# Kernel tuning notes

Hardware: AMD Instinct MI355X
Metric: run time of the kernel (lower is better)

## Reference

```python
import jax, jax.numpy as jnp
import numpy as np

EPS = 1e-5  # InstanceNorm2d default eps


def setup_inputs() -> dict:
    key = jax.random.key(0)
    ks = jax.random.split(key, 5)
    B, T, C, N, H = 4, 8, 256, 196, 4
    s = 1.0 / np.sqrt(C)
    return {
        "emb": jax.random.normal(ks[0], (B, T, C, N), dtype=jnp.float32),
        "Wq": jax.random.normal(ks[1], (H, C, C), dtype=jnp.float32) * s,
        "Wk": jax.random.normal(ks[2], (H, C, C), dtype=jnp.float32) * s,
        "Wv": jax.random.normal(ks[3], (H, C, C), dtype=jnp.float32) * s,
        "Wo": jax.random.normal(ks[4], (C, C), dtype=jnp.float32) * s,
    }


def reference(emb, Wq, Wk, Wv, Wo):
    B, T, C, N = emb.shape
    S = T * N  # KV_size
    # emb.permute(0,1,3,2).view(B, T*N, C)
    x = jnp.transpose(emb, (0, 1, 3, 2)).reshape(B, S, C)
    # per-head full-width Linear projections (nn.Linear: y = x @ W.T)
    Q = jnp.einsum("bsc,hdc->bhsd", x, Wq)  # [B,H,S,C]
    K = jnp.einsum("bsc,hdc->bhsd", x, Wk)
    V = jnp.einsum("bsc,hdc->bhsd", x, Wv)
    scores = jnp.einsum("bhsd,bhtd->bhst", Q, K) / jnp.sqrt(jnp.float32(S))
    # InstanceNorm2d over each [S,S] map per (batch, head), no affine, biased var
    mean = jnp.mean(scores, axis=(-2, -1), keepdims=True)
    var = jnp.var(scores, axis=(-2, -1), keepdims=True)
    normed = (scores - mean) * jax.lax.rsqrt(var + EPS)
    probs = jax.nn.softmax(normed, axis=-1)  # attn_dropout: eval-mode identity
    ctx = jnp.einsum("bhst,bhtd->bhsd", probs, V)  # [B,H,S,C]
    ctx = jnp.mean(ctx, axis=1)  # mean over heads -> [B,S,C]
    O1 = jnp.einsum("bsc,dc->bsd", ctx, Wo)  # out Linear; proj_dropout identity
    # .view(-1, num_frames, num_channels, num_patches) on contiguous [B, T*N, C]
    return O1.reshape(B, T, C, N)
```

## Files before the change

kernel.cpp:

```cpp
#include <hip/hip_runtime.h>
#include <stdint.h>

typedef unsigned short u16;

#define Bb 4
#define Hh 4
#define Tt 8
#define Cc 256
#define NP 196
#define Ss 1568
#define SCALE_S 0.0252538136f
#define LST 32
#define KC 64
#define NCH 25
#define LPP 72

typedef __attribute__((ext_vector_type(4))) float floatx4;
typedef __attribute__((ext_vector_type(8))) short shortx8;

__device__ __forceinline__ float bf2f(u16 u) {
    union { unsigned u; float f; } v; v.u = ((unsigned)u) << 16; return v.f;
}
__device__ __forceinline__ u16 f2bf(float f) {
    union { float f; unsigned u; } v; v.f = f;
    unsigned r = v.u + 0x7FFFu + ((v.u >> 16) & 1u);
    return (u16)(r >> 16);
}

typedef const __attribute__((address_space(1))) void* gas1_t;
typedef __attribute__((address_space(3))) void* las3_t;
__device__ __forceinline__ void gld16(const void* g, void* l) {
    __builtin_amdgcn_global_load_lds((gas1_t)g, (las3_t)l, 16, 0, 0);
}

__global__ __launch_bounds__(256) void k_convall(const float* __restrict__ Wq,
                                                 const float* __restrict__ Wk,
                                                 const float* __restrict__ Wv,
                                                 const float* __restrict__ Wo,
                                                 u16* __restrict__ dst) {
    const int NW = Hh * Cc * Cc;
    int i = blockIdx.x * 256 + threadIdx.x;
    float v;
    if (i < NW) v = Wq[i];
    else if (i < 2 * NW) v = Wk[i - NW];
    else if (i < 3 * NW) v = Wv[i - 2 * NW];
    else if (i < 3 * NW + Cc * Cc) v = Wo[i - 3 * NW];
    else return;
    dst[i] = f2bf(v);
}

__device__ __forceinline__ void mfma_step(const u16* As, const u16* Bs, int lane,
                                          int wm, int wn, floatx4 acc[4][4]) {
    const int r15 = lane & 15;
    const int kq  = (lane >> 4) << 3;
    shortx8 a[4], b[4];
#pragma unroll
    for (int i = 0; i < 4; ++i)
        a[i] = *(const shortx8*)(As + (wm * 64 + i * 16 + r15) * LST + kq);
#pragma unroll
    for (int j = 0; j < 4; ++j)
        b[j] = *(const shortx8*)(Bs + (wn * 64 + j * 16 + r15) * LST + kq);
#pragma unroll
    for (int i = 0; i < 4; ++i)
#pragma unroll
        for (int j = 0; j < 4; ++j)
            acc[i][j] = __builtin_amdgcn_mfma_f32_16x16x32_bf16(a[i], b[j], acc[i][j], 0, 0, 0);
}

__device__ __forceinline__ void gemm_bt_core(const u16* A, const u16* Bm, int lda, int ldb,
                                             int mbase, int mlast, int nbase, int nlast,
                                             int KD, u16* As, u16* Bs, floatx4 acc[4][4]) {
    int tid = threadIdx.x;
    int lane = tid & 63, wave = tid >> 6, wm = wave >> 1, wn = wave & 1;
    int row0 = tid >> 2, row1 = 64 + row0;
    int cole = (tid & 3) << 3;
    int ga0 = mbase + row0; ga0 = ga0 <= mlast ? ga0 : mlast;
    int ga1 = mbase + row1; ga1 = ga1 <= mlast ? ga1 : mlast;
    int gb0 = nbase + row0; gb0 = gb0 <= nlast ? gb0 : nlast;
    int gb1 = nbase + row1; gb1 = gb1 <= nlast ? gb1 : nlast;
    const u16* pa0 = A  + (size_t)ga0 * lda + cole;
    const u16* pa1 = A  + (size_t)ga1 * lda + cole;
    const u16* pb0 = Bm + (size_t)gb0 * ldb + cole;
    const u16* pb1 = Bm + (size_t)gb1 * ldb + cole;
    shortx8 xa0 = *(const shortx8*)(pa0),      xa1 = *(const shortx8*)(pa1);
    shortx8 xb0 = *(const shortx8*)(pb0),      xb1 = *(const shortx8*)(pb1);
    shortx8 ya0 = *(const shortx8*)(pa0 + 32), ya1 = *(const shortx8*)(pa1 + 32);
    shortx8 yb0 = *(const shortx8*)(pb0 + 32), yb1 = *(const shortx8*)(pb1 + 32);
    for (int k0 = 0; k0 < KD; k0 += 64) {
        __syncthreads();
        *(shortx8*)(As + row0 * LST + cole) = xa0;
        *(shortx8*)(As + row1 * LST + cole) = xa1;
        *(shortx8*)(Bs + row0 * LST + cole) = xb0;
        *(shortx8*)(Bs + row1 * LST + cole) = xb1;
        int kp = k0 + 64;
        if (kp < KD) {
            xa0 = *(const shortx8*)(pa0 + kp); xa1 = *(const shortx8*)(pa1 + kp);
            xb0 = *(const shortx8*)(pb0 + kp); xb1 = *(const shortx8*)(pb1 + kp);
        }
        __syncthreads();
        mfma_step(As, Bs, lane, wm, wn, acc);
        if (k0 + 32 < KD) {
            __syncthreads();
            *(shortx8*)(As + row0 * LST + cole) = ya0;
            *(shortx8*)(As + row1 * LST + cole) = ya1;
            *(shortx8*)(Bs + row0 * LST + cole) = yb0;
            *(shortx8*)(Bs + row1 * LST + cole) = yb1;
            int kq2 = k0 + 96;
            if (kq2 < KD) {
                ya0 = *(const shortx8*)(pa0 + kq2); ya1 = *(const shortx8*)(pa1 + kq2);
                yb0 = *(const shortx8*)(pb0 + kq2); yb1 = *(const shortx8*)(pb1 + kq2);
            }
            __syncthreads();
            mfma_step(As, Bs, lane, wm, wn, acc);
        }
    }
}

__global__ void k_transpose(const float* __restrict__ emb, u16* __restrict__ x) {
    __shared__ u16 tile[32][33];
    int bt = blockIdx.z;
    int c0 = blockIdx.y * 32, n0 = blockIdx.x * 32;
    const float* src = emb + (size_t)bt * Cc * NP;
#pragma unroll
    for (int rr = 0; rr < 32; rr += 8) {
        int c = c0 + threadIdx.y + rr;
        int n = n0 + threadIdx.x;
        u16 v = 0;
        if (n < NP) v = f2bf(src[(size_t)c * NP + n]);
        tile[threadIdx.y + rr][threadIdx.x] = v;
    }
    __syncthreads();
    int b = bt / Tt, t = bt % Tt;
    u16* dst = x + ((size_t)b * Ss + (size_t)t * NP) * Cc;
#pragma unroll
    for (int rr = 0; rr < 32; rr += 8) {
        int n = n0 + threadIdx.y + rr;
        int c = c0 + threadIdx.x;
        if (n < NP) dst[(size_t)n * Cc + c] = tile[threadIdx.x][threadIdx.y + rr];
    }
}

__global__ __launch_bounds__(256) void k_qkv(const u16* __restrict__ x,
                                             const u16* __restrict__ Wall,
                                             u16* __restrict__ Q, u16* __restrict__ Kb,
                                             u16* __restrict__ Vt, u16* __restrict__ Qt,
                                             u16* __restrict__ Kt, float* __restrict__ cs) {
    __shared__ __align__(16) u16 As[128 * LST], Bs[128 * LST];
    floatx4 acc[4][4];
#pragma unroll
    for (int i = 0; i < 4; ++i)
#pragma unroll
        for (int j = 0; j < 4; ++j) acc[i][j] = (floatx4)(0.f);
    int z = blockIdx.z;
    int qkv = z >> 4, bh = z & 15, b = bh >> 2, h = bh & 3;
    const u16* A = x + (size_t)b * Ss * Cc;
    const u16* W = Wall + (size_t)qkv * Hh * Cc * Cc + (size_t)h * Cc * Cc;
    int mbase = blockIdx.y * 128, nbase = blockIdx.x * 128;
    gemm_bt_core(A, W, Cc, Cc, mbase, Ss - 1, nbase, Cc - 1, Cc, As, Bs, acc);

    int tid = threadIdx.x, lane = tid & 63, wave = tid >> 6, wm = wave >> 1, wn = wave & 1;
    int rq = (lane >> 4) << 2, cn = lane & 15;
    if (qkv < 2) {
        u16* outr = (qkv == 0 ? Q : Kb) + (size_t)bh * Ss * Cc;
        u16* outt = (qkv == 0 ? Qt : Kt) + (size_t)bh * Cc * Ss;
#pragma unroll
        for (int i = 0; i < 4; ++i) {
            int m0 = mbase + wm * 64 + i * 16 + rq;
#pragma unroll
            for (int j = 0; j < 4; ++j) {
                int n = nbase + wn * 64 + j * 16 + cn;
                ushort4 v;
                v.x = f2bf(acc[i][j][0]); v.y = f2bf(acc[i][j][1]);
                v.z = f2bf(acc[i][j][2]); v.w = f2bf(acc[i][j][3]);
#pragma unroll
                for (int r = 0; r < 4; ++r) {
                    int m = m0 + r;
                    if (m < Ss) outr[(size_t)m * Cc + n] = f2bf(acc[i][j][r]);
                }
                if (m0 < Ss) *(ushort4*)(outt + (size_t)n * Ss + m0) = v;
            }
        }
#pragma unroll
        for (int j = 0; j < 4; ++j) {
            float s = 0.f;
#pragma unroll
            for (int i = 0; i < 4; ++i) {
                int m0 = mbase + wm * 64 + i * 16 + rq;
#pragma unroll
                for (int r = 0; r < 4; ++r)
                    if (m0 + r < Ss) s += acc[i][j][r];
            }
            s += __shfl_xor(s, 16); s += __shfl_xor(s, 32);
            if ((lane >> 4) == 0) {
                int n = nbase + wn * 64 + j * 16 + cn;
                atomicAdd(&cs[(size_t)(qkv * 16 + bh) * Cc + n], s);
            }
        }
    } else {
        u16* out = Vt + (size_t)bh * Cc * Ss;
#pragma unroll
        for (int i = 0; i < 4; ++i) {
            int m0 = mbase + wm * 64 + i * 16 + rq;
            if (m0 < Ss) {
#pragma unroll
                for (int j = 0; j < 4; ++j) {
                    int n = nbase + wn * 64 + j * 16 + cn;
                    ushort4 v;
                    v.x = f2bf(acc[i][j][0]); v.y = f2bf(acc[i][j][1]);
                    v.z = f2bf(acc[i][j][2]); v.w = f2bf(acc[i][j][3]);
                    *(ushort4*)(out + (size_t)n * Ss + m0) = v;
                }
            }
        }
    }
}

__global__ __launch_bounds__(256) void k_gram(const u16* __restrict__ Qt,
                                              const u16* __restrict__ Kt,
                                              float* __restrict__ Gp) {
    __shared__ __align__(16) u16 As[128 * LST], Bs[128 * LST];
    floatx4 acc[4][4];
#pragma unroll
    for (int i = 0; i < 4; ++i)
#pragma unroll
        for (int j = 0; j < 4; ++j) acc[i][j] = (floatx4)(0.f);
    int z = blockIdx.z;
    int qk = z >> 6, rem = z & 63, bh = rem >> 2, ks = rem & 3;
    int kstart = ks * 384;
    int klen = (ks == 3) ? 416 : 384;
    const u16* T = (qk ? Kt : Qt) + (size_t)bh * Cc * Ss + kstart;
    int mbase = blockIdx.y * 128, nbase = blockIdx.x * 128;
    gemm_bt_core(T, T, Ss, Ss, mbase, Cc - 1, nbase, Cc - 1, klen, As, Bs, acc);

    int tid = threadIdx.x, lane = tid & 63, wave = tid >> 6, wm = wave >> 1, wn = wave & 1;
    int rq = (lane >> 4) << 2, cn = lane & 15;
    float* o = Gp + (size_t)z * (Cc * Cc);
#pragma unroll
    for (int i = 0; i < 4; ++i) {
        int mb = mbase + wm * 64 + i * 16 + rq;
#pragma unroll
        for (int j = 0; j < 4; ++j) {
            int n = nbase + wn * 64 + j * 16 + cn;
#pragma unroll
            for (int r = 0; r < 4; ++r)
                o[(size_t)(mb + r) * Cc + n] = acc[i][j][r];
        }
    }
}

__global__ __launch_bounds__(256) void k_dot(const float* __restrict__ Gp,
                                             const float* __restrict__ cs,
                                             float* __restrict__ stats) {
    __shared__ float red[4];
    int bh = blockIdx.y;
    int tid = threadIdx.x, lane = tid & 63, wave = tid >> 6;
    const size_t CC2 = (size_t)Cc * Cc;
    size_t bq = (size_t)(bh << 2) * CC2;
    size_t bk = (size_t)(64 + (bh << 2)) * CC2;
    float s2 = 0.f;
    int e0 = blockIdx.x * 8192;
#pragma unroll 4
    for (int i = 0; i < 32; ++i) {
        int e = e0 + i * 256 + tid;
        float gq = Gp[bq + e] + Gp[bq + CC2 + e] + Gp[bq + 2 * CC2 + e] + Gp[bq + 3 * CC2 + e];
        float gk = Gp[bk + e] + Gp[bk + CC2 + e] + Gp[bk + 2 * CC2 + e] + Gp[bk + 3 * CC2 + e];
        s2 += gq * gk;
    }
#pragma unroll
    for (int mk = 1; mk <= 32; mk <<= 1) s2 += __shfl_xor(s2, mk);
    __syncthreads();
    if (lane == 0) red[wave] = s2;
    __syncthreads();
    if (tid == 0)
        atomicAdd(&stats[bh * 4 + 1], (red[0] + red[1] + red[2] + red[3]) * (SCALE_S * SCALE_S));
    if (blockIdx.x == 0) {
        float s1 = cs[(size_t)bh * Cc + tid] * cs[(size_t)(16 + bh) * Cc + tid];
#pragma unroll
        for (int mk = 1; mk <= 32; mk <<= 1) s1 += __shfl_xor(s1, mk);
        __syncthreads();
        if (lane == 0) red[wave] = s1;
        __syncthreads();
        if (tid == 0)
            atomicAdd(&stats[bh * 4 + 0], (red[0] + red[1] + red[2] + red[3]) * SCALE_S);
    }
}

__global__ __launch_bounds__(256, 2) void k_fused(const u16* __restrict__ Q,
                                                  const u16* __restrict__ Kb,
                                                  const u16* __restrict__ Vt,
                                                  const float* __restrict__ stats,
                                                  float* __restrict__ ctxm) {
    extern __shared__ u16 smem[];
    u16* Kls = smem;
    u16* Ps  = smem + 32768;
    float* rsp = (float*)((char*)smem + 74752);
    float* rs2 = rsp + 128;

    int L = blockIdx.x;
    int xcd = L & 7, idx = L >> 3;
    int bh = xcd + 8 * (idx / 25);
    int mt = idx % 25;
    int mbase = mt * 64;

    float inv  = 1.f / ((float)Ss * (float)Ss);
    float mean = stats[bh * 4] * inv;
    float var  = fmaxf(stats[bh * 4 + 1] * inv - mean * mean, 0.f);
    float istd = rsqrtf(var + 1e-5f);
    float aa   = istd * 1.44269504f;
    float aas  = aa * SCALE_S;
    float bb   = -mean * aa;

    const u16* Qp = Q  + (size_t)bh * Ss * Cc;
    const u16* Kp = Kb + (size_t)bh * Ss * Cc;
    const u16* Vp = Vt + (size_t)bh * Cc * Ss;

    int tid = threadIdx.x, lane = tid & 63, wv = tid >> 6;
    const int r15 = lane & 15;
    const int g   = lane >> 4;
    const int kq  = g << 3;
    const int prow = g << 2;
    const int wqm = wv >> 1, wqn = wv & 1;
    const int swz = (r15 & 7) << 4;

    shortx8 Qa[8][2];
#pragma unroll
    for (int kk = 0; kk < 8; ++kk)
#pragma unroll
        for (int i = 0; i < 2; ++i) {
            int row = mbase + wqm * 32 + i * 16 + r15;
            row = row < Ss ? row : Ss - 1;
            Qa[kk][i] = *(const shortx8*)(Qp + (size_t)row * Cc + kk * 32 + kq);
        }

#pragma unroll
    for (int pass = 0; pass < 8; ++pass) {
        int rb = pass * 4 + wv;
        int r2 = rb * 2 + (lane >> 5);
        int colb = (lane & 31) << 4;
        int scol = colb ^ ((r2 & 7) << 4);
        gld16((const char*)Kp + (size_t)r2 * 512 + scol, Kls + rb * 512);
    }
    __syncthreads();

    floatx4 acc[4][4];
#pragma unroll
    for (int i = 0; i < 4; ++i)
#pragma unroll
        for (int j = 0; j < 4; ++j) acc[i][j] = (floatx4)(0.f);
    float rsum[2][4];
    rsum[0][0] = rsum[0][1] = rsum[0][2] = rsum[0][3] = 0.f;
    rsum[1][0] = rsum[1][1] = rsum[1][2] = rsum[1][3] = 0.f;

    int cur = 0;
    for (int c = 0; c < NCH; ++c) {
        int kc = c * KC;
        const u16* Kcur = Kls + cur * 16384;
        if (c + 1 < NCH) {
            int kc1 = kc + KC;
            u16* Knxt = Kls + (cur ^ 1) * 16384;
#pragma unroll
            for (int pass = 0; pass < 8; ++pass) {
                int rb = pass * 4 + wv;
                int r2 = rb * 2 + (lane >> 5);
                int colb = (lane & 31) << 4;
                int scol = colb ^ ((r2 & 7) << 4);
                int grow = kc1 + r2; grow = grow < Ss ? grow : 0;
                gld16((const char*)Kp + (size_t)grow * 512 + scol, Knxt + rb * 512);
            }
        }
        shortx8 vf[2][4];
#pragma unroll
        for (int kk2 = 0; kk2 < 2; ++kk2)
#pragma unroll
            for (int nj = 0; nj < 4; ++nj) {
                int vr = wv * 64 + nj * 16 + r15;
                int vc = kc + kk2 * 32 + kq;
                vc = (vc + 8 <= Ss) ? vc : 0;
                vf[kk2][nj] = *(const shortx8*)(Vp + (size_t)vr * Ss + vc);
            }
        floatx4 accs[2][2];
        accs[0][0] = (floatx4)(0.f); accs[0][1] = (floatx4)(0.f);
        accs[1][0] = (floatx4)(0.f); accs[1][1] = (floatx4)(0.f);
        const int cb = g << 4;
#pragma unroll
        for (int kk = 0; kk < 8; ++kk) {
            int cbx = (kk * 64 + cb) ^ swz;
            shortx8 b0 = *(const shortx8*)((const char*)Kcur + (wqn * 32 + r15) * 512 + cbx);
            shortx8 b1 = *(const shortx8*)((const char*)Kcur + (wqn * 32 + 16 + r15) * 512 + cbx);
            accs[0][0] = __builtin_amdgcn_mfma_f32_16x16x32_bf16(Qa[kk][0], b0, accs[0][0], 0, 0, 0);
            accs[1][0] = __builtin_amdgcn_mfma_f32_16x16x32_bf16(Qa[kk][1], b0, accs[1][0], 0, 0, 0);
            accs[0][1] = __builtin_amdgcn_mfma_f32_16x16x32_bf16(Qa[kk][0], b1, accs[0][1], 0, 0, 0);
            accs[1][1] = __builtin_amdgcn_mfma_f32_16x16x32_bf16(Qa[kk][1], b1, accs[1][1], 0, 0, 0);
        }
#pragma unroll
        for (int j = 0; j < 2; ++j) {
            bool valid = (kc + wqn * 32 + j * 16 + r15) < Ss;
#pragma unroll
            for (int i = 0; i < 2; ++i)
#pragma unroll
                for (int r = 0; r < 4; ++r) {
                    float ex = valid ? exp2f(accs[i][j][r] * aas + bb) : 0.f;
                    accs[i][j][r] = ex;
                    rsum[i][r] += ex;
                }
        }
        __syncthreads();
#pragma unroll
        for (int i = 0; i < 2; ++i)
#pragma unroll
            for (int j = 0; j < 2; ++j)
#pragma unroll
                for (int r = 0; r < 4; ++r)
                    Ps[(wqm * 32 + i * 16 + prow + r) * LPP + wqn * 32 + j * 16 + r15] =
                        f2bf(accs[i][j][r]);
        __syncthreads();
#pragma unroll
        for (int kk2 = 0; kk2 < 2; ++kk2) {
            shortx8 pa_[4];
#pragma unroll
            for (int i2 = 0; i2 < 4; ++i2)
                pa_[i2] = *(const shortx8*)(Ps + (i2 * 16 + r15) * LPP + kk2 * 32 + kq);
#pragma unroll
            for (int i2 = 0; i2 < 4; ++i2)
#pragma unroll
                for (int nj = 0; nj < 4; ++nj)
                    acc[i2][nj] = __builtin_amdgcn_mfma_f32_16x16x32_bf16(
                        pa_[i2], vf[kk2][nj], acc[i2][nj], 0, 0, 0);
        }
        cur ^= 1;
    }

#pragma unroll
    for (int i = 0; i < 2; ++i)
#pragma unroll
        for (int r = 0; r < 4; ++r) {
            float v = rsum[i][r];
            v += __shfl_xor(v, 1); v += __shfl_xor(v, 2);
            v += __shfl_xor(v, 4); v += __shfl_xor(v, 8);
            if (r15 == 0) rsp[wqn * 64 + wqm * 32 + i * 16 + prow + r] = v;
        }
    __syncthreads();
    if (tid < 64) rs2[tid] = rsp[tid] + rsp[64 + tid];
    __syncthreads();

    int b = bh >> 2;
    float* outp = ctxm + (size_t)b * Ss * Cc;
#pragma unroll
    for (int i2 = 0; i2 < 4; ++i2) {
#pragma unroll
        for (int r = 0; r < 4; ++r) {
            int ml = i2 * 16 + prow + r;
            int m = mbase + ml;
            if (m < Ss) {
                float invs = 0.25f / rs2[ml];
#pragma unroll
                for (int nj = 0; nj < 4; ++nj) {
                    int n = wv * 64 + nj * 16 + r15;
                    atomicAdd(&outp[(size_t)m * Cc + n], acc[i2][nj][r] * invs);
                }
            }
        }
    }
}

__global__ __launch_bounds__(256) void k_out(const float* __restrict__ ctxm,
                                             const u16* __restrict__ Wo, float* __restrict__ out) {
    __shared__ __align__(16) u16 As[128 * LST], Bs[128 * LST];
    floatx4 acc[4][4];
#pragma unroll
    for (int i = 0; i < 4; ++i)
#pragma unroll
        for (int j = 0; j < 4; ++j) acc[i][j] = (floatx4)(0.f);
    int b = blockIdx.z;
    const float* A = ctxm + (size_t)b * Ss * Cc;
    int mbase = blockIdx.y * 128, nbase = blockIdx.x * 128;
    int tid = threadIdx.x, lane = tid & 63, wave = tid >> 6, wm = wave >> 1, wn = wave & 1;
    int row0 = tid >> 2, row1 = 64 + row0;
    int cole = (tid & 3) << 3;
    int ga0 = mbase + row0; ga0 = ga0 <= Ss - 1 ? ga0 : Ss - 1;
    int ga1 = mbase + row1; ga1 = ga1 <= Ss - 1 ? ga1 : Ss - 1;
    const float* pa0 = A + (size_t)ga0 * Cc + cole;
    const float* pa1 = A + (size_t)ga1 * Cc + cole;
    const u16* pb0 = Wo + (size_t)(nbase + row0 <= Cc - 1 ? nbase + row0 : Cc - 1) * Cc + cole;
    const u16* pb1 = Wo + (size_t)(nbase + row1 <= Cc - 1 ? nbase + row1 : Cc - 1) * Cc + cole;
    float4 a00 = *(const float4*)(pa0), a01 = *(const float4*)(pa0 + 4);
    float4 a10 = *(const float4*)(pa1), a11 = *(const float4*)(pa1 + 4);
    shortx8 vb0 = *(const shortx8*)(pb0);
    shortx8 vb1 = *(const shortx8*)(pb1);
    for (int k0 = 0; k0 < Cc; k0 += 32) {
        shortx8 o0, o1;
        o0[0] = (short)f2bf(a00.x); o0[1] = (short)f2bf(a00.y); o0[2] = (short)f2bf(a00.z); o0[3] = (short)f2bf(a00.w);
        o0[4] = (short)f2bf(a01.x); o0[5] = (short)f2bf(a01.y); o0[6] = (short)f2bf(a01.z); o0[7] = (short)f2bf(a01.w);
        o1[0] = (short)f2bf(a10.x); o1[1] = (short)f2bf(a10.y); o1[2] = (short)f2bf(a10.z); o1[3] = (short)f2bf(a10.w);
        o1[4] = (short)f2bf(a11.x); o1[5] = (short)f2bf(a11.y); o1[6] = (short)f2bf(a11.z); o1[7] = (short)f2bf(a11.w);
        __syncthreads();
        *(shortx8*)(As + row0 * LST + cole) = o0;
        *(shortx8*)(As + row1 * LST + cole) = o1;
        *(shortx8*)(Bs + row0 * LST + cole) = vb0;
        *(shortx8*)(Bs + row1 * LST + cole) = vb1;
        int k1 = k0 + 32;
        if (k1 < Cc) {
            a00 = *(const float4*)(pa0 + k1); a01 = *(const float4*)(pa0 + k1 + 4);
            a10 = *(const float4*)(pa1 + k1); a11 = *(const float4*)(pa1 + k1 + 4);
            vb0 = *(const shortx8*)(pb0 + k1);
            vb1 = *(const shortx8*)(pb1 + k1);
        }
        __syncthreads();
        mfma_step(As, Bs, lane, wm, wn, acc);
    }
    int rq = (lane >> 4) << 2, cn = lane & 15;
    float* o = out + (size_t)b * Ss * Cc;
#pragma unroll
    for (int i = 0; i < 4; ++i) {
        int mb = mbase + wm * 64 + i * 16 + rq;
#pragma unroll
        for (int j = 0; j < 4; ++j) {
            int n = nbase + wn * 64 + j * 16 + cn;
#pragma unroll
            for (int r = 0; r < 4; ++r) {
                int m = mb + r;
                if (m < Ss) o[(size_t)m * Cc + n] = acc[i][j][r];
            }
        }
    }
}

extern "C" void kernel_launch(void* const* d_in, const int* in_sizes, int n_in,
                              void* d_out, int out_size, void* d_ws, size_t ws_size,
                              hipStream_t stream) {
    const float* emb = (const float*)d_in[0];
    float* out = (float*)d_out;

    char* ws = (char*)d_ws;
    size_t off = 0;
    auto alloc = [&](size_t bytes) -> void* {
        void* p = ws + off;
        off = (off + bytes + 255) & ~(size_t)255;
        return p;
    };
    float* stats = (float*)alloc(16 * 4 * sizeof(float));
    u16* Wall = (u16*)alloc((size_t)(3 * Hh + 1) * Cc * Cc * 2);
    u16* x    = (u16*)alloc((size_t)Bb * Ss * Cc * 2);
    u16* Q    = (u16*)alloc((size_t)Bb * Hh * Ss * Cc * 2);
    u16* Kb   = (u16*)alloc((size_t)Bb * Hh * Ss * Cc * 2);
    u16* Vt   = (u16*)alloc((size_t)Bb * Hh * Ss * Cc * 2);
    u16* Qt   = (u16*)alloc((size_t)Bb * Hh * Ss * Cc * 2);
    u16* Kt   = (u16*)alloc((size_t)Bb * Hh * Ss * Cc * 2);
    float* ctxm = (float*)alloc((size_t)Bb * Ss * Cc * 4);
    float* Gp   = (float*)alloc((size_t)128 * Cc * Cc * 4);
    float* cs   = (float*)alloc((size_t)32 * Cc * 4);
    u16* Woc  = Wall + (size_t)3 * Hh * Cc * Cc;

    hipMemsetAsync(stats, 0, 16 * 4 * sizeof(float), stream);
    hipMemsetAsync(ctxm, 0, (size_t)Bb * Ss * Cc * 4, stream);
    hipMemsetAsync(cs, 0, (size_t)32 * Cc * 4, stream);

    k_convall<<<dim3(3328), dim3(256), 0, stream>>>((const float*)d_in[1], (const float*)d_in[2],
                                                    (const float*)d_in[3], (const float*)d_in[4], Wall);
    k_transpose<<<dim3(7, 8, 32), dim3(32, 8), 0, stream>>>(emb, x);
    k_qkv<<<dim3(2, 13, 48), dim3(256), 0, stream>>>(x, Wall, Q, Kb, Vt, Qt, Kt, cs);
    k_gram<<<dim3(2, 2, 128), dim3(256), 0, stream>>>(Qt, Kt, Gp);
    k_dot<<<dim3(8, 16), dim3(256), 0, stream>>>(Gp, cs, stats);
    k_fused<<<dim3(400), dim3(256), 75520, stream>>>(Q, Kb, Vt, stats, ctxm);
    k_out<<<dim3(2, 13, 4), dim3(256), 0, stream>>>(ctxm, Woc, out);
}
```

Before: 214.3 us.

## Compute transposed scores so each wave owns its P tile and drops block barriers

The QK^T MFMA now computes S^T (K as the A operand), so each wave holds a 32x32 probability tile and writes it into its own private LDS slab. It then runs P·V over all 256 output columns using its own 32 KV columns, which removes the two block-wide barriers around the shared P buffer. V fragments are now loaded from global memory inside the loop, 16 per chunk, instead of being prefetched. This doubles the per-wave accumulator registers (2x16 tiles), and the two waves sharing a row block now both atomically add partial results, which doubles the atomic traffic to ctxm.

```diff
diff --git a/kernel.cpp b/kernel.cpp
--- a/kernel.cpp
+++ b/kernel.cpp
@@ -13,7 +13,6 @@
 #define LST 32
 #define KC 64
 #define NCH 25
-#define LPP 72
 
 typedef __attribute__((ext_vector_type(4))) float floatx4;
 typedef __attribute__((ext_vector_type(8))) short shortx8;
@@ -292,8 +291,8 @@
                                                   float* __restrict__ ctxm) {
     extern __shared__ u16 smem[];
     u16* Kls = smem;
-    u16* Ps  = smem + 32768;
-    float* rsp = (float*)((char*)smem + 74752);
+    u16* Pw  = smem + 32768;
+    float* rsp = (float*)(smem + 32768 + 5120);
     float* rs2 = rsp + 128;
 
     int L = blockIdx.x;
@@ -318,9 +317,9 @@
     const int r15 = lane & 15;
     const int g   = lane >> 4;
     const int kq  = g << 3;
-    const int prow = g << 2;
     const int wqm = wv >> 1, wqn = wv & 1;
     const int swz = (r15 & 7) << 4;
+    u16* Pwv = Pw + wv * 1280;
 
     shortx8 Qa[8][2];
 #pragma unroll
@@ -340,20 +339,18 @@
         int scol = colb ^ ((r2 & 7) << 4);
         gld16((const char*)Kp + (size_t)r2 * 512 + scol, Kls + rb * 512);
     }
-    __syncthreads();
-
-    floatx4 acc[4][4];
-#pragma unroll
-    for (int i = 0; i < 4; ++i)
-#pragma unroll
-        for (int j = 0; j < 4; ++j) acc[i][j] = (floatx4)(0.f);
-    float rsum[2][4];
-    rsum[0][0] = rsum[0][1] = rsum[0][2] = rsum[0][3] = 0.f;
-    rsum[1][0] = rsum[1][1] = rsum[1][2] = rsum[1][3] = 0.f;
+
+    floatx4 acc[2][16];
+#pragma unroll
+    for (int u = 0; u < 2; ++u)
+#pragma unroll
+        for (int j = 0; j < 16; ++j) acc[u][j] = (floatx4)(0.f);
+    float ru[2] = {0.f, 0.f};
 
     int cur = 0;
     for (int c = 0; c < NCH; ++c) {
         int kc = c * KC;
+        __syncthreads();
         const u16* Kcur = Kls + cur * 16384;
         if (c + 1 < NCH) {
             int kc1 = kc + KC;
@@ -368,16 +365,6 @@
                 gld16((const char*)Kp + (size_t)grow * 512 + scol, Knxt + rb * 512);
             }
         }
-        shortx8 vf[2][4];
-#pragma unroll
-        for (int kk2 = 0; kk2 < 2; ++kk2)
-#pragma unroll
-            for (int nj = 0; nj < 4; ++nj) {
-                int vr = wv * 64 + nj * 16 + r15;
-                int vc = kc + kk2 * 32 + kq;
-                vc = (vc + 8 <= Ss) ? vc : 0;
-                vf[kk2][nj] = *(const shortx8*)(Vp + (size_t)vr * Ss + vc);
-            }
         floatx4 accs[2][2];
         accs[0][0] = (floatx4)(0.f); accs[0][1] = (floatx4)(0.f);
         accs[1][0] = (floatx4)(0.f); accs[1][1] = (floatx4)(0.f);
@@ -385,60 +372,57 @@
 #pragma unroll
         for (int kk = 0; kk < 8; ++kk) {
             int cbx = (kk * 64 + cb) ^ swz;
-            shortx8 b0 = *(const shortx8*)((const char*)Kcur + (wqn * 32 + r15) * 512 + cbx);
-            shortx8 b1 = *(const shortx8*)((const char*)Kcur + (wqn * 32 + 16 + r15) * 512 + cbx);
-            accs[0][0] = __builtin_amdgcn_mfma_f32_16x16x32_bf16(Qa[kk][0], b0, accs[0][0], 0, 0, 0);
-            accs[1][0] = __builtin_amdgcn_mfma_f32_16x16x32_bf16(Qa[kk][1], b0, accs[1][0], 0, 0, 0);
-            accs[0][1] = __builtin_amdgcn_mfma_f32_16x16x32_bf16(Qa[kk][0], b1, accs[0][1], 0, 0, 0);
-            accs[1][1] = __builtin_amdgcn_mfma_f32_16x16x32_bf16(Qa[kk][1], b1, accs[1][1], 0, 0, 0);
-        }
-#pragma unroll
-        for (int j = 0; j < 2; ++j) {
-            bool valid = (kc + wqn * 32 + j * 16 + r15) < Ss;
-#pragma unroll
-            for (int i = 0; i < 2; ++i)
+            shortx8 k0 = *(const shortx8*)((const char*)Kcur + (wqn * 32 + r15) * 512 + cbx);
+            shortx8 k1 = *(const shortx8*)((const char*)Kcur + (wqn * 32 + 16 + r15) * 512 + cbx);
+            accs[0][0] = __builtin_amdgcn_mfma_f32_16x16x32_bf16(k0, Qa[kk][0], accs[0][0], 0, 0, 0);
+            accs[0][1] = __builtin_amdgcn_mfma_f32_16x16x32_bf16(k0, Qa[kk][1], accs[0][1], 0, 0, 0);
+            accs[1][0] = __builtin_amdgcn_mfma_f32_16x16x32_bf16(k1, Qa[kk][0], accs[1][0], 0, 0, 0);
+            accs[1][1] = __builtin_amdgcn_mfma_f32_16x16x32_bf16(k1, Qa[kk][1], accs[1][1], 0, 0, 0);
+        }
+#pragma unroll
+        for (int t = 0; t < 2; ++t)
+#pragma unroll
+            for (int u = 0; u < 2; ++u) {
+                float p[4];
 #pragma unroll
                 for (int r = 0; r < 4; ++r) {
-                    float ex = valid ? exp2f(accs[i][j][r] * aas + bb) : 0.f;
-                    accs[i][j][r] = ex;
-                    rsum[i][r] += ex;
+                    int kvg = kc + wqn * 32 + t * 16 + 4 * g + r;
+                    p[r] = (kvg < Ss) ? exp2f(accs[t][u][r] * aas + bb) : 0.f;
+                    ru[u] += p[r];
                 }
-        }
-        __syncthreads();
-#pragma unroll
-        for (int i = 0; i < 2; ++i)
-#pragma unroll
-            for (int j = 0; j < 2; ++j)
-#pragma unroll
-                for (int r = 0; r < 4; ++r)
-                    Ps[(wqm * 32 + i * 16 + prow + r) * LPP + wqn * 32 + j * 16 + r15] =
-                        f2bf(accs[i][j][r]);
-        __syncthreads();
-#pragma unroll
-        for (int kk2 = 0; kk2 < 2; ++kk2) {
-            shortx8 pa_[4];
-#pragma unroll
-            for (int i2 = 0; i2 < 4; ++i2)
-                pa_[i2] = *(const shortx8*)(Ps + (i2 * 16 + r15) * LPP + kk2 * 32 + kq);
-#pragma unroll
-            for (int i2 = 0; i2 < 4; ++i2)
-#pragma unroll
-                for (int nj = 0; nj < 4; ++nj)
-                    acc[i2][nj] = __builtin_amdgcn_mfma_f32_16x16x32_bf16(
-                        pa_[i2], vf[kk2][nj], acc[i2][nj], 0, 0, 0);
+                unsigned d0 = (unsigned)f2bf(p[0]) | ((unsigned)f2bf(p[1]) << 16);
+                unsigned d1 = (unsigned)f2bf(p[2]) | ((unsigned)f2bf(p[3]) << 16);
+                char* base = (char*)Pwv + (u * 16 + r15) * 80 + t * 32 + 8 * g;
+                *(unsigned*)(base) = d0;
+                *(unsigned*)(base + 4) = d1;
+            }
+        shortx8 PA[2];
+#pragma unroll
+        for (int u = 0; u < 2; ++u)
+            PA[u] = *(const shortx8*)((const char*)Pwv + (u * 16 + r15) * 80 + 16 * g);
+#pragma unroll
+        for (int j = 0; j < 16; ++j) {
+            int vr = j * 16 + r15;
+            int vc = kc + wqn * 32 + kq;
+            vc = (vc + 8 <= Ss) ? vc : 0;
+            shortx8 bV = *(const shortx8*)(Vp + (size_t)vr * Ss + vc);
+            acc[0][j] = __builtin_amdgcn_mfma_f32_16x16x32_bf16(PA[0], bV, acc[0][j], 0, 0, 0);
+            acc[1][j] = __builtin_amdgcn_mfma_f32_16x16x32_bf16(PA[1], bV, acc[1][j], 0, 0, 0);
         }
         cur ^= 1;
     }
 
 #pragma unroll
-    for (int i = 0; i < 2; ++i)
-#pragma unroll
-        for (int r = 0; r < 4; ++r) {
-            float v = rsum[i][r];
-            v += __shfl_xor(v, 1); v += __shfl_xor(v, 2);
-            v += __shfl_xor(v, 4); v += __shfl_xor(v, 8);
-            if (r15 == 0) rsp[wqn * 64 + wqm * 32 + i * 16 + prow + r] = v;
-        }
+    for (int u = 0; u < 2; ++u) {
+        ru[u] += __shfl_xor(ru[u], 16);
+        ru[u] += __shfl_xor(ru[u], 32);
+    }
+    __syncthreads();
+    if (g == 0) {
+#pragma unroll
+        for (int u = 0; u < 2; ++u)
+            rsp[wqn * 64 + wqm * 32 + u * 16 + r15] = ru[u];
+    }
     __syncthreads();
     if (tid < 64) rs2[tid] = rsp[tid] + rsp[64 + tid];
     __syncthreads();
@@ -446,17 +430,17 @@
     int b = bh >> 2;
     float* outp = ctxm + (size_t)b * Ss * Cc;
 #pragma unroll
-    for (int i2 = 0; i2 < 4; ++i2) {
+    for (int u = 0; u < 2; ++u) {
 #pragma unroll
         for (int r = 0; r < 4; ++r) {
-            int ml = i2 * 16 + prow + r;
+            int ml = wqm * 32 + u * 16 + 4 * g + r;
             int m = mbase + ml;
             if (m < Ss) {
                 float invs = 0.25f / rs2[ml];
 #pragma unroll
-                for (int nj = 0; nj < 4; ++nj) {
-                    int n = wv * 64 + nj * 16 + r15;
-                    atomicAdd(&outp[(size_t)m * Cc + n], acc[i2][nj][r] * invs);
+                for (int j = 0; j < 16; ++j) {
+                    int n = j * 16 + r15;
+                    atomicAdd(&outp[(size_t)m * Cc + n], acc[u][j][r] * invs);
                 }
             }
         }
@@ -561,6 +545,6 @@
     k_qkv<<<dim3(2, 13, 48), dim3(256), 0, stream>>>(x, Wall, Q, Kb, Vt, Qt, Kt, cs);
     k_gram<<<dim3(2, 2, 128), dim3(256), 0, stream>>>(Qt, Kt, Gp);
     k_dot<<<dim3(8, 16), dim3(256), 0, stream>>>(Gp, cs, stats);
-    k_fused<<<dim3(400), dim3(256), 75520, stream>>>(Q, Kb, Vt, stats, ctxm);
+    k_fused<<<dim3(400), dim3(256), 76544, stream>>>(Q, Kb, Vt, stats, ctxm);
     k_out<<<dim3(2, 13, 4), dim3(256), 0, stream>>>(ctxm, Woc, out);
 }
```

After: 392.1 us. 1.83x slower.
